# Kernel optimization log

Measured on AMD Instinct MI355X. Metric: run time of the kernel, lower is better.

The kernel has to match this reference:

```python
import jax, jax.numpy as jnp
import numpy as np

N_HEAD = 8
NEG = -1e9


def setup_inputs() -> dict:
    key = jax.random.key(0)
    ks = jax.random.split(key, 12)
    B, S, D = 16, 512, 512
    query = jax.random.normal(ks[0], (B, S, D), dtype=jnp.float32)
    inputs = jax.random.normal(ks[1], (B, S, D), dtype=jnp.float32)
    # repetition-count matrix (nonnegative ints, used via log10(x+1))
    ren_mat = jax.random.randint(ks[2], (B, S, S), 0, 10).astype(jnp.float32)
    # signed time-gap matrix (used via exp(-|t|))
    timestamp = jax.random.normal(ks[3], (B, S, S), dtype=jnp.float32) * 3.0
    # causal future mask: True above the diagonal (k=1)
    mask = jnp.triu(jnp.ones((1, S, S), dtype=bool), k=1)
    scale = 0.02
    Wq = jax.random.normal(ks[4], (D, D), dtype=jnp.float32) * scale
    Wk = jax.random.normal(ks[5], (D, D), dtype=jnp.float32) * scale
    Wv = jax.random.normal(ks[6], (D, D), dtype=jnp.float32) * scale
    Wo = jax.random.normal(ks[7], (D, D), dtype=jnp.float32) * scale
    W1 = jax.random.normal(ks[8], (D, D), dtype=jnp.float32) * scale
    bq = jnp.zeros((D,), jnp.float32); bk = jnp.zeros((D,), jnp.float32)
    bv = jnp.zeros((D,), jnp.float32); bo = jnp.zeros((D,), jnp.float32)
    b1 = jnp.zeros((D,), jnp.float32)
    ln_g = jnp.ones((D,), jnp.float32); ln_b = jnp.zeros((D,), jnp.float32)
    l1 = jax.random.uniform(ks[9], (1,), dtype=jnp.float32)  # nn.Parameter(torch.rand(1))
    gammas = jax.random.normal(ks[10], (N_HEAD, 1, 1), dtype=jnp.float32) * 0.1
    return {"query": query, "inputs": inputs, "ren_mat": ren_mat,
            "timestamp": timestamp, "mask": mask,
            "Wq": Wq, "bq": bq, "Wk": Wk, "bk": bk, "Wv": Wv, "bv": bv,
            "Wo": Wo, "bo": bo, "W1": W1, "b1": b1,
            "ln_g": ln_g, "ln_b": ln_b, "l1": l1, "gammas": gammas}


def reference(query, inputs, ren_mat, timestamp, mask,
              Wq, bq, Wk, bk, Wv, bv, Wo, bo, W1, b1, ln_g, ln_b, l1, gammas):
    B, S, D = inputs.shape
    H = N_HEAD
    hd = D // H

    def proj(x, W, b):
        # nn.Linear: x @ W.T + b, then split heads -> (B, H, S, hd)
        return (x @ W.T + b).reshape(B, S, H, hd).transpose(0, 2, 1, 3)

    q = proj(inputs, Wq, bq)
    k = proj(inputs, Wk, bk)
    v = proj(inputs, Wv, bv)

    m = mask[:, None]  # (1,1,S,S)
    # softplus(gammas) is computed in the original but unused by the math
    _ = jax.nn.softplus(gammas)

    scores = jnp.einsum('bhqd,bhkd->bhqk', q, k) / np.float32(np.sqrt(hd))
    prob_attn = jax.nn.softmax(jnp.where(m, NEG, scores), axis=-1)

    # memory-decay branch: log10 recency + exp time-decay, softmax-fused
    ren_feat = jnp.where(m, NEG, jnp.log10(ren_mat[:, None] + 1.0))   # (B,1,S,S)
    time_feat = jnp.where(m, NEG, jnp.exp(-jnp.abs(timestamp[:, None])))
    mem_attn = jax.nn.softmax(ren_feat + time_feat, axis=-1)          # (B,1,S,S)

    l = l1[0]
    p = (1.0 - l) * prob_attn + l * mem_attn  # broadcast over heads (== repeat)

    out = jnp.einsum('bhqk,bhkd->bhqd', p, v)
    out = out.transpose(0, 2, 1, 3).reshape(B, S, D)
    out = out @ Wo.T + bo            # MHA lin_out
    out = out + (out @ W1.T + b1)    # SMFE residual (dropout off in eval)
    # LayerNorm (biased variance, eps=1e-5)
    mu = out.mean(-1, keepdims=True)
    var = jnp.mean((out - mu) ** 2, axis=-1, keepdims=True)
    out = (out - mu) / jnp.sqrt(var + 1e-5) * ln_g + ln_b
    return out
```

## Files before the change

kernel.cpp:

```cpp
#include <hip/hip_runtime.h>
#include <hip/hip_bf16.h>

constexpr int B = 16, S = 512, D = 512, H = 8, HD = 64;
constexpr int BS = B * S;

typedef __attribute__((ext_vector_type(8))) short bf16x8;
typedef __attribute__((ext_vector_type(4))) float f32x4;

#define DEVI __device__ __forceinline__

DEVI bf16x8 ldbf8(const __hip_bfloat16* p) {
    return *reinterpret_cast<const bf16x8*>(p);
}

DEVI unsigned short bfbits(float f) {
    __hip_bfloat16 h = __float2bfloat16(f);
    return __builtin_bit_cast(unsigned short, h);
}

DEVI void gload_lds16(const void* g, void* l) {
    __builtin_amdgcn_global_load_lds((const __attribute__((address_space(1))) void*)g,
                                     (__attribute__((address_space(3))) void*)l, 16, 0, 0);
}

__global__ __launch_bounds__(256) void cvt_kernel(const float* __restrict__ src,
                                                  __hip_bfloat16* __restrict__ dst,
                                                  int n4) {
    int i = blockIdx.x * 256 + threadIdx.x;
    if (i >= n4) return;
    float4 v = reinterpret_cast<const float4*>(src)[i];
    unsigned int lo = (unsigned int)bfbits(v.x) | ((unsigned int)bfbits(v.y) << 16);
    unsigned int hi = (unsigned int)bfbits(v.z) | ((unsigned int)bfbits(v.w) << 16);
    uint2 o; o.x = lo; o.y = hi;
    reinterpret_cast<uint2*>(dst)[i] = o;
}

__global__ __launch_bounds__(256) void wcvt_kernel(const float* __restrict__ s0,
                                                   const float* __restrict__ s1,
                                                   const float* __restrict__ s2,
                                                   const float* __restrict__ s3,
                                                   const float* __restrict__ s4,
                                                   __hip_bfloat16* __restrict__ dst) {
    int idx = blockIdx.x * 256 + threadIdx.x;
    int wsel = idx >> 16;
    int off = idx & 65535;
    const float* s;
    switch (wsel) {
        case 0: s = s0; break;
        case 1: s = s1; break;
        case 2: s = s2; break;
        case 3: s = s3; break;
        default: s = s4; break;
    }
    float4 v = reinterpret_cast<const float4*>(s)[off];
    unsigned int lo = (unsigned int)bfbits(v.x) | ((unsigned int)bfbits(v.y) << 16);
    unsigned int hi = (unsigned int)bfbits(v.z) | ((unsigned int)bfbits(v.w) << 16);
    uint2 o; o.x = lo; o.y = hi;
    reinterpret_cast<uint2*>(dst)[idx] = o;
}

__global__ __launch_bounds__(256) void mem_attn_kernel(const float* __restrict__ ren,
                                                       const float* __restrict__ ts,
                                                       __hip_bfloat16* __restrict__ mem) {
    int tid = threadIdx.x;
    int w = tid >> 6, l = tid & 63;
    int row = blockIdx.x * 4 + w;
    int qr = row & (S - 1);
    size_t base = (size_t)row * S + l * 8;
    float f[8];
    bool active = (l * 8 <= qr);
    if (active) {
        float4 r0 = *reinterpret_cast<const float4*>(ren + base);
        float4 r1 = *reinterpret_cast<const float4*>(ren + base + 4);
        float4 t0 = *reinterpret_cast<const float4*>(ts + base);
        float4 t1 = *reinterpret_cast<const float4*>(ts + base + 4);
        float rv[8] = {r0.x, r0.y, r0.z, r0.w, r1.x, r1.y, r1.z, r1.w};
        float tv[8] = {t0.x, t0.y, t0.z, t0.w, t1.x, t1.y, t1.z, t1.w};
#pragma unroll
        for (int j = 0; j < 8; ++j) {
            int c = l * 8 + j;
            f[j] = (c <= qr) ? (__log2f(rv[j] + 1.0f) * 0.3010299957f + __expf(-fabsf(tv[j])))
                             : -3.0e38f;
        }
    } else {
#pragma unroll
        for (int j = 0; j < 8; ++j) f[j] = -3.0e38f;
    }
    float m = -3.0e38f;
#pragma unroll
    for (int j = 0; j < 8; ++j) m = fmaxf(m, f[j]);
#pragma unroll
    for (int off = 32; off >= 1; off >>= 1) m = fmaxf(m, __shfl_xor(m, off));
    float s = 0.f;
#pragma unroll
    for (int j = 0; j < 8; ++j) { float e = __expf(f[j] - m); f[j] = e; s += e; }
#pragma unroll
    for (int off = 32; off >= 1; off >>= 1) s += __shfl_xor(s, off);
    float inv = 1.0f / s;
    bf16x8 o;
#pragma unroll
    for (int j = 0; j < 8; ++j) o[j] = (short)bfbits(f[j] * inv);
    *reinterpret_cast<bf16x8*>(mem + base) = o;
}

__global__ __launch_bounds__(256) void gemm_qkv(const __hip_bfloat16* __restrict__ A,
                                                const __hip_bfloat16* __restrict__ Wqkv,
                                                const float* __restrict__ bq,
                                                const float* __restrict__ bk,
                                                const float* __restrict__ bv,
                                                __hip_bfloat16* __restrict__ q_out,
                                                __hip_bfloat16* __restrict__ k_out,
                                                __hip_bfloat16* __restrict__ vT_out) {
    constexpr int K = 512;
    int tid = threadIdx.x;
    int wv = tid >> 6, l = tid & 63;
    int wR = wv >> 1, wC = wv & 1;
    int lr = l & 15, lg = l >> 4;
    int mat = blockIdx.y >> 2;
    int rowBase = blockIdx.x * 128 + wR * 64;
    int colBase = (blockIdx.y & 3) * 128 + wC * 64;
    const float* bias = (mat == 0) ? bq : (mat == 1) ? bk : bv;
    const __hip_bfloat16* W = Wqkv + (size_t)mat * D * D;
    const __hip_bfloat16* Ab = A + (size_t)(rowBase + lr) * K + lg * 8;
    const __hip_bfloat16* Wb = W + (size_t)(colBase + lr) * K + lg * 8;

    f32x4 acc[4][4];
#pragma unroll
    for (int m = 0; m < 4; ++m)
#pragma unroll
        for (int n = 0; n < 4; ++n) acc[m][n] = (f32x4){0.f, 0.f, 0.f, 0.f};

    for (int kk = 0; kk < K; kk += 32) {
        bf16x8 a[4], b[4];
#pragma unroll
        for (int m = 0; m < 4; ++m) a[m] = ldbf8(Ab + (size_t)m * 16 * K + kk);
#pragma unroll
        for (int n = 0; n < 4; ++n) b[n] = ldbf8(Wb + (size_t)n * 16 * K + kk);
#pragma unroll
        for (int m = 0; m < 4; ++m)
#pragma unroll
            for (int n = 0; n < 4; ++n)
                acc[m][n] = __builtin_amdgcn_mfma_f32_16x16x32_bf16(a[m], b[n], acc[m][n], 0, 0, 0);
    }

#pragma unroll
    for (int n = 0; n < 4; ++n) {
        int col = colBase + n * 16 + lr;
        float bs = bias[col];
#pragma unroll
        for (int m = 0; m < 4; ++m) {
#pragma unroll
            for (int i = 0; i < 4; ++i) {
                int row = rowBase + m * 16 + lg * 4 + i;
                float val = acc[m][n][i] + bs;
                int b_ = row >> 9, s_ = row & 511, h_ = col >> 6, d_ = col & 63;
                if (mat == 2) {
                    vT_out[(((size_t)(b_ * 8 + h_) * 64 + d_) << 9) + s_] = __float2bfloat16(val);
                } else {
                    __hip_bfloat16* o = (mat == 0) ? q_out : k_out;
                    o[(((size_t)(b_ * 8 + h_) * 512 + s_) << 6) + d_] = __float2bfloat16(val);
                }
            }
        }
    }
}

template <int MODE>
__global__ __launch_bounds__(256) void gemm_bt(const __hip_bfloat16* __restrict__ A,
                                               const __hip_bfloat16* __restrict__ W,
                                               const float* __restrict__ bias,
                                               float* __restrict__ outf,
                                               __hip_bfloat16* __restrict__ outb,
                                               const float* __restrict__ resid) {
    constexpr int K = 512;
    int tid = threadIdx.x;
    int wv = tid >> 6, l = tid & 63;
    int wR = wv >> 1, wC = wv & 1;
    int lr = l & 15, lg = l >> 4;
    int rowBase = blockIdx.x * 128 + wR * 64;
    int colBase = blockIdx.y * 128 + wC * 64;
    const __hip_bfloat16* Ab = A + (size_t)(rowBase + lr) * K + lg * 8;
    const __hip_bfloat16* Wb = W + (size_t)(colBase + lr) * K + lg * 8;

    f32x4 acc[4][4];
#pragma unroll
    for (int m = 0; m < 4; ++m)
#pragma unroll
        for (int n = 0; n < 4; ++n) acc[m][n] = (f32x4){0.f, 0.f, 0.f, 0.f};

    for (int kk = 0; kk < K; kk += 32) {
        bf16x8 a[4], b[4];
#pragma unroll
        for (int m = 0; m < 4; ++m) a[m] = ldbf8(Ab + (size_t)m * 16 * K + kk);
#pragma unroll
        for (int n = 0; n < 4; ++n) b[n] = ldbf8(Wb + (size_t)n * 16 * K + kk);
#pragma unroll
        for (int m = 0; m < 4; ++m)
#pragma unroll
            for (int n = 0; n < 4; ++n)
                acc[m][n] = __builtin_amdgcn_mfma_f32_16x16x32_bf16(a[m], b[n], acc[m][n], 0, 0, 0);
    }

#pragma unroll
    for (int n = 0; n < 4; ++n) {
        int col = colBase + n * 16 + lr;
        float bs = bias[col];
#pragma unroll
        for (int m = 0; m < 4; ++m) {
#pragma unroll
            for (int i = 0; i < 4; ++i) {
                int row = rowBase + m * 16 + lg * 4 + i;
                float val = acc[m][n][i] + bs;
                size_t idx = (size_t)row * 512 + col;
                if constexpr (MODE == 2) {
                    outf[idx] = val;
                    outb[idx] = __float2bfloat16(val);
                } else {
                    outf[idx] = val + resid[idx];
                }
            }
        }
    }
}

__global__ __launch_bounds__(256) void gemm_memv(const __hip_bfloat16* __restrict__ A,
                                                 const __hip_bfloat16* __restrict__ VT,
                                                 __hip_bfloat16* __restrict__ outb) {
    int tid = threadIdx.x;
    int wv = tid >> 6, l = tid & 63;
    int wR = wv >> 1, wC = wv & 1;
    int lr = l & 15, lg = l >> 4;
    int rowBase = blockIdx.x * 128 + wR * 64;
    int colBase = blockIdx.y * 128 + wC * 64;
    int b = rowBase >> 9;
    int h = colBase >> 6;
    int klim = ((blockIdx.x & 3) + 1) * 128;

    const __hip_bfloat16* Ab = A + (size_t)(rowBase + lr) * 512 + lg * 8;
    const __hip_bfloat16* Wb = VT + ((size_t)(b * 8 + h) * 64 + lr) * 512 + lg * 8;

    f32x4 acc[4][4];
#pragma unroll
    for (int m = 0; m < 4; ++m)
#pragma unroll
        for (int n = 0; n < 4; ++n) acc[m][n] = (f32x4){0.f, 0.f, 0.f, 0.f};

    for (int kk = 0; kk < klim; kk += 32) {
        bf16x8 a[4], bb[4];
#pragma unroll
        for (int m = 0; m < 4; ++m) a[m] = ldbf8(Ab + (size_t)m * 16 * 512 + kk);
#pragma unroll
        for (int n = 0; n < 4; ++n) bb[n] = ldbf8(Wb + (size_t)n * 16 * 512 + kk);
#pragma unroll
        for (int m = 0; m < 4; ++m)
#pragma unroll
            for (int n = 0; n < 4; ++n)
                acc[m][n] = __builtin_amdgcn_mfma_f32_16x16x32_bf16(a[m], bb[n], acc[m][n], 0, 0, 0);
    }

#pragma unroll
    for (int n = 0; n < 4; ++n) {
        int col = colBase + n * 16 + lr;
#pragma unroll
        for (int m = 0; m < 4; ++m)
#pragma unroll
            for (int i = 0; i < 4; ++i) {
                int row = rowBase + m * 16 + lg * 4 + i;
                outb[(size_t)row * 512 + col] = __float2bfloat16(acc[m][n][i]);
            }
    }
}

__global__ __launch_bounds__(256, 3) void attn2_kernel(const __hip_bfloat16* __restrict__ Q,
                                                       const __hip_bfloat16* __restrict__ Km,
                                                       const __hip_bfloat16* __restrict__ VT,
                                                       const __hip_bfloat16* __restrict__ memv,
                                                       const float* __restrict__ l1,
                                                       __hip_bfloat16* __restrict__ outb) {
    __shared__ short lds[20480];
    short* Kb = lds;
    short* Vb = lds + 8192;
    int tid = threadIdx.x;
    int w = tid >> 6, l = tid & 63;
    int lr = l & 15, lg = l >> 4;
    int blk = blockIdx.x;
    int bh = blk & 127, qt = blk >> 7;
    int b = bh >> 3, h = bh & 7;
    int q0 = qt * 64;
    int nt = qt + 1;
    short* Pw = lds + 16384 + w * 1024;

    const char* Kg = (const char*)Km + (size_t)bh * 65536;
    const char* Vg = (const char*)VT + (size_t)bh * 65536;

    int o0 = w * 64 + l;
    const __hip_bfloat16* qp = Q + ((size_t)bh * 512 + q0 + w * 16 + lr) * 64 + lg * 8;
    bf16x8 qa0 = ldbf8(qp), qa1 = ldbf8(qp + 32);
    float lam = l1[0];

#pragma unroll
    for (int c = 0; c < 2; ++c) {
        int o = c * 256 + o0;
        int r = o >> 3, c16 = o & 7;
        int sw = ((c16 ^ (r & 7)) << 4);
        gload_lds16(Kg + r * 128 + sw, (char*)Kb + o * 16);
        gload_lds16(Vg + r * 1024 + sw, (char*)Vb + o * 16);
    }
    __syncthreads();

    f32x4 acc2[4];
#pragma unroll
    for (int n = 0; n < 4; ++n) acc2[n] = (f32x4){0.f, 0.f, 0.f, 0.f};
    float mrun[4] = {-3e38f, -3e38f, -3e38f, -3e38f};
    float psum[4] = {0.f, 0.f, 0.f, 0.f};

    for (int t = 0; t < nt; ++t) {
        if (t + 1 < nt) {
#pragma unroll
            for (int c = 0; c < 2; ++c) {
                int o = c * 256 + o0;
                int r = o >> 3, c16 = o & 7;
                int sw = ((c16 ^ (r & 7)) << 4);
                gload_lds16(Kg + (t + 1) * 8192 + r * 128 + sw,
                            (char*)Kb + ((t + 1) & 1) * 8192 + o * 16);
                gload_lds16(Vg + r * 1024 + (t + 1) * 128 + sw,
                            (char*)Vb + ((t + 1) & 1) * 8192 + o * 16);
            }
        }
        const short* kb = Kb + (t & 1) * 4096;
        const short* vb = Vb + (t & 1) * 4096;

        f32x4 s4[4];
#pragma unroll
        for (int j = 0; j < 4; ++j) {
            int row = j * 16 + lr;
            int sw = row & 7;
            bf16x8 k0 = *reinterpret_cast<const bf16x8*>(kb + row * 64 + ((lg ^ sw) << 3));
            bf16x8 k1 = *reinterpret_cast<const bf16x8*>(kb + row * 64 + (((4 + lg) ^ sw) << 3));
            f32x4 cc = {0.f, 0.f, 0.f, 0.f};
            cc = __builtin_amdgcn_mfma_f32_16x16x32_bf16(qa0, k0, cc, 0, 0, 0);
            cc = __builtin_amdgcn_mfma_f32_16x16x32_bf16(qa1, k1, cc, 0, 0, 0);
            s4[j] = cc;
        }

        if (t == nt - 1) {
#pragma unroll
            for (int j = 0; j < 4; ++j) {
                int col = t * 64 + j * 16 + lr;
#pragma unroll
                for (int i = 0; i < 4; ++i) {
                    int rowg = q0 + w * 16 + lg * 4 + i;
                    s4[j][i] = (col <= rowg) ? s4[j][i] * 0.125f : -3e38f;
                }
            }
        } else {
#pragma unroll
            for (int j = 0; j < 4; ++j)
#pragma unroll
                for (int i = 0; i < 4; ++i) s4[j][i] *= 0.125f;
        }

        float tmax[4];
#pragma unroll
        for (int i = 0; i < 4; ++i)
            tmax[i] = fmaxf(fmaxf(s4[0][i], s4[1][i]), fmaxf(s4[2][i], s4[3][i]));
#pragma unroll
        for (int off = 1; off < 16; off <<= 1)
#pragma unroll
            for (int i = 0; i < 4; ++i) tmax[i] = fmaxf(tmax[i], __shfl_xor(tmax[i], off));

        float e[4][4];
#pragma unroll
        for (int i = 0; i < 4; ++i) {
            float mnew = fmaxf(mrun[i], tmax[i]);
            float sc = __expf(mrun[i] - mnew);
            mrun[i] = mnew;
            float ps = 0.f;
#pragma unroll
            for (int j = 0; j < 4; ++j) {
                float ee = __expf(s4[j][i] - mnew);
                e[j][i] = ee;
                ps += ee;
            }
            psum[i] = psum[i] * sc + ps;
#pragma unroll
            for (int n = 0; n < 4; ++n) acc2[n][i] *= sc;
        }

#pragma unroll
        for (int j = 0; j < 4; ++j)
#pragma unroll
            for (int i = 0; i < 4; ++i) {
                int rr = lg * 4 + i;
                int cc = j * 16 + lr;
                Pw[rr * 64 + (cc ^ ((rr & 7) << 3))] = (short)bfbits(e[j][i]);
            }

#pragma unroll
        for (int ksub = 0; ksub < 2; ++ksub) {
            bf16x8 pa = *reinterpret_cast<const bf16x8*>(
                Pw + lr * 64 + (((ksub * 4 + lg) ^ (lr & 7)) << 3));
#pragma unroll
            for (int n = 0; n < 4; ++n) {
                int d = n * 16 + lr;
                bf16x8 vf = *reinterpret_cast<const bf16x8*>(
                    vb + d * 64 + (((ksub * 4 + lg) ^ (d & 7)) << 3));
                acc2[n] = __builtin_amdgcn_mfma_f32_16x16x32_bf16(pa, vf, acc2[n], 0, 0, 0);
            }
        }
        __syncthreads();
    }

#pragma unroll
    for (int off = 1; off < 16; off <<= 1)
#pragma unroll
        for (int i = 0; i < 4; ++i) psum[i] += __shfl_xor(psum[i], off);
    float rinv[4];
#pragma unroll
    for (int i = 0; i < 4; ++i) rinv[i] = (1.0f - lam) / psum[i];

    const __hip_bfloat16* mvp = memv + ((size_t)b * 512 + q0 + w * 16 + lg * 4) * 512 + h * 64;
    __hip_bfloat16* op = outb + ((size_t)b * 512 + q0 + w * 16 + lg * 4) * 512 + h * 64;
#pragma unroll
    for (int n = 0; n < 4; ++n)
#pragma unroll
        for (int i = 0; i < 4; ++i) {
            float mv = __bfloat162float(mvp[(size_t)i * 512 + n * 16 + lr]);
            op[(size_t)i * 512 + n * 16 + lr] =
                __float2bfloat16(acc2[n][i] * rinv[i] + lam * mv);
        }
}

__global__ __launch_bounds__(256) void ln_kernel(float* __restrict__ io,
                                                 const float* __restrict__ g,
                                                 const float* __restrict__ bb) {
    int tid = threadIdx.x;
    int w = tid >> 6, l = tid & 63;
    size_t row = (size_t)blockIdx.x * 4 + w;
    float* p = io + row * 512 + l * 8;
    float4 x0 = *reinterpret_cast<float4*>(p);
    float4 x1 = *reinterpret_cast<float4*>(p + 4);
    float xs[8] = {x0.x, x0.y, x0.z, x0.w, x1.x, x1.y, x1.z, x1.w};
    float s = 0.f;
#pragma unroll
    for (int j = 0; j < 8; ++j) s += xs[j];
#pragma unroll
    for (int off = 32; off >= 1; off >>= 1) s += __shfl_xor(s, off);
    float mu = s * (1.0f / 512.0f);
    float vs = 0.f;
#pragma unroll
    for (int j = 0; j < 8; ++j) { float d = xs[j] - mu; vs += d * d; }
#pragma unroll
    for (int off = 32; off >= 1; off >>= 1) vs += __shfl_xor(vs, off);
    float rstd = rsqrtf(vs * (1.0f / 512.0f) + 1e-5f);
    const float4 g0 = *reinterpret_cast<const float4*>(g + l * 8);
    const float4 g1 = *reinterpret_cast<const float4*>(g + l * 8 + 4);
    const float4 b0 = *reinterpret_cast<const float4*>(bb + l * 8);
    const float4 b1 = *reinterpret_cast<const float4*>(bb + l * 8 + 4);
    float gs[8] = {g0.x, g0.y, g0.z, g0.w, g1.x, g1.y, g1.z, g1.w};
    float bs[8] = {b0.x, b0.y, b0.z, b0.w, b1.x, b1.y, b1.z, b1.w};
    float ys[8];
#pragma unroll
    for (int j = 0; j < 8; ++j) ys[j] = (xs[j] - mu) * rstd * gs[j] + bs[j];
    float4 y0 = make_float4(ys[0], ys[1], ys[2], ys[3]);
    float4 y1 = make_float4(ys[4], ys[5], ys[6], ys[7]);
    *reinterpret_cast<float4*>(p) = y0;
    *reinterpret_cast<float4*>(p + 4) = y1;
}

extern "C" void kernel_launch(void* const* d_in, const int* in_sizes, int n_in,
                              void* d_out, int out_size, void* d_ws, size_t ws_size,
                              hipStream_t stream) {
    const float* inputs = (const float*)d_in[1];
    const float* ren    = (const float*)d_in[2];
    const float* ts     = (const float*)d_in[3];
    const float* Wq = (const float*)d_in[5];
    const float* bq = (const float*)d_in[6];
    const float* Wk = (const float*)d_in[7];
    const float* bk = (const float*)d_in[8];
    const float* Wv = (const float*)d_in[9];
    const float* bv = (const float*)d_in[10];
    const float* Wo = (const float*)d_in[11];
    const float* bo = (const float*)d_in[12];
    const float* W1 = (const float*)d_in[13];
    const float* b1 = (const float*)d_in[14];
    const float* ln_g = (const float*)d_in[15];
    const float* ln_b = (const float*)d_in[16];
    const float* l1   = (const float*)d_in[17];
    float* out = (float*)d_out;

    char* ws = (char*)d_ws;
    __hip_bfloat16* in_bf = (__hip_bfloat16*)(ws + 0);
    __hip_bfloat16* ao_bf = (__hip_bfloat16*)(ws + 0);
    __hip_bfloat16* wq_bf = (__hip_bfloat16*)(ws + 8388608);
    __hip_bfloat16* wo_bf = (__hip_bfloat16*)(ws + 9961472);
    __hip_bfloat16* w1_bf = (__hip_bfloat16*)(ws + 10485760);
    __hip_bfloat16* q_bf  = (__hip_bfloat16*)(ws + 11010048);
    __hip_bfloat16* o1_bf = (__hip_bfloat16*)(ws + 11010048);
    __hip_bfloat16* k_bf  = (__hip_bfloat16*)(ws + 19398656);
    __hip_bfloat16* vT_bf = (__hip_bfloat16*)(ws + 27787264);
    __hip_bfloat16* mem_bf = (__hip_bfloat16*)(ws + 36175872);
    float*          out1_f = (float*)(ws + 36175872);
    __hip_bfloat16* memv_bf = (__hip_bfloat16*)(ws + 69730304);

    cvt_kernel<<<4096, 256, 0, stream>>>(inputs, in_bf, BS * D / 4);
    wcvt_kernel<<<1280, 256, 0, stream>>>(Wq, Wk, Wv, Wo, W1, wq_bf);

    gemm_qkv<<<dim3(64, 12), 256, 0, stream>>>(in_bf, wq_bf, bq, bk, bv, q_bf, k_bf, vT_bf);

    mem_attn_kernel<<<BS / 4, 256, 0, stream>>>(ren, ts, mem_bf);

    gemm_memv<<<dim3(64, 4), 256, 0, stream>>>(mem_bf, vT_bf, memv_bf);

    attn2_kernel<<<1024, 256, 0, stream>>>(q_bf, k_bf, vT_bf, memv_bf, l1, ao_bf);

    gemm_bt<2><<<dim3(64, 4), 256, 0, stream>>>(ao_bf, wo_bf, bo, out1_f, o1_bf, nullptr);

    gemm_bt<3><<<dim3(64, 4), 256, 0, stream>>>(o1_bf, w1_bf, b1, out, nullptr, out1_f);

    ln_kernel<<<BS / 4, 256, 0, stream>>>(out, ln_g, ln_b);
}
```

Baseline: 287.9 us.

## Stage GEMM tiles through double-buffered LDS and vectorize epilogue stores via swizzled LDS

Replaces the direct-from-global MFMA operand loads in the QKV, memv, out-projection and FFN GEMMs with a shared mainloop. It stages 128x32 A and W tiles into double-buffered LDS using global_load_lds, so all four waves share the data instead of each fetching its own. The QKV and memv epilogues now write results through an XOR-swizzled LDS scratch and emit 16-byte vector stores, including the transposed V layout, instead of scattered 2-byte stores. This adds LDS usage and a barrier per k-step, which may reduce occupancy.

Result: faster. 257.3 us (-10.6%).

```diff
diff --git a/kernel.cpp b/kernel.cpp
--- a/kernel.cpp
+++ b/kernel.cpp
@@ -103,26 +103,68 @@
     *reinterpret_cast<bf16x8*>(mem + base) = o;
 }
 
-__global__ __launch_bounds__(256) void gemm_qkv(const __hip_bfloat16* __restrict__ A,
-                                                const __hip_bfloat16* __restrict__ Wqkv,
-                                                const float* __restrict__ bq,
-                                                const float* __restrict__ bk,
-                                                const float* __restrict__ bv,
-                                                __hip_bfloat16* __restrict__ q_out,
-                                                __hip_bfloat16* __restrict__ k_out,
-                                                __hip_bfloat16* __restrict__ vT_out) {
-    constexpr int K = 512;
-    int tid = threadIdx.x;
-    int wv = tid >> 6, l = tid & 63;
-    int wR = wv >> 1, wC = wv & 1;
-    int lr = l & 15, lg = l >> 4;
+
+DEVI void stage_tiles(const __hip_bfloat16* __restrict__ A,
+                      const __hip_bfloat16* __restrict__ W,
+                      int rowBase, int colBase, int kt, short* ldsbuf, int tid) {
+#pragma unroll
+    for (int c = 0; c < 2; ++c) {
+        int o = c * 256 + tid;
+        int row = o & 127, ch = o >> 7;
+        gload_lds16(A + (size_t)(rowBase + row) * 512 + kt * 32 + ch * 8,
+                    (char*)ldsbuf + o * 16);
+        gload_lds16(W + (size_t)(colBase + row) * 512 + kt * 32 + ch * 8,
+                    (char*)ldsbuf + 8192 + o * 16);
+    }
+}
+
+DEVI void gemm_mainloop(const __hip_bfloat16* __restrict__ A,
+                        const __hip_bfloat16* __restrict__ W,
+                        int rowBase, int colBase, int ktiles,
+                        short* lds, f32x4 (&acc)[4][4]) {
+    int tid = threadIdx.x;
+    int w = tid >> 6, l = tid & 63, lr = l & 15, lg = l >> 4;
+    int wR = w >> 1, wC = w & 1;
+    stage_tiles(A, W, rowBase, colBase, 0, lds, tid);
+    __syncthreads();
+    for (int t = 0; t < ktiles; ++t) {
+        if (t + 1 < ktiles)
+            stage_tiles(A, W, rowBase, colBase, t + 1, lds + ((t + 1) & 1) * 8192, tid);
+        const short* ab = lds + (t & 1) * 8192;
+        const short* bb = ab + 4096;
+        bf16x8 af[4], bfr[4];
+#pragma unroll
+        for (int m = 0; m < 4; ++m)
+            af[m] = *reinterpret_cast<const bf16x8*>(ab + (lg * 128 + wR * 64 + m * 16 + lr) * 8);
+#pragma unroll
+        for (int n = 0; n < 4; ++n)
+            bfr[n] = *reinterpret_cast<const bf16x8*>(bb + (lg * 128 + wC * 64 + n * 16 + lr) * 8);
+#pragma unroll
+        for (int m = 0; m < 4; ++m)
+#pragma unroll
+            for (int n = 0; n < 4; ++n)
+                acc[m][n] = __builtin_amdgcn_mfma_f32_16x16x32_bf16(af[m], bfr[n], acc[m][n], 0, 0, 0);
+        __syncthreads();
+    }
+}
+
+__global__ __launch_bounds__(256) void gemm_qkv_s(const __hip_bfloat16* __restrict__ A,
+                                                  const __hip_bfloat16* __restrict__ Wqkv,
+                                                  const float* __restrict__ bq,
+                                                  const float* __restrict__ bk,
+                                                  const float* __restrict__ bv,
+                                                  __hip_bfloat16* __restrict__ q_out,
+                                                  __hip_bfloat16* __restrict__ k_out,
+                                                  __hip_bfloat16* __restrict__ vT_out) {
+    __shared__ short lds[16384];
+    int tid = threadIdx.x;
+    int w = tid >> 6, l = tid & 63, lr = l & 15, lg = l >> 4;
+    int wR = w >> 1, wC = w & 1;
     int mat = blockIdx.y >> 2;
-    int rowBase = blockIdx.x * 128 + wR * 64;
-    int colBase = (blockIdx.y & 3) * 128 + wC * 64;
+    int rowBase = blockIdx.x * 128;
+    int colBase = (blockIdx.y & 3) * 128;
     const float* bias = (mat == 0) ? bq : (mat == 1) ? bk : bv;
-    const __hip_bfloat16* W = Wqkv + (size_t)mat * D * D;
-    const __hip_bfloat16* Ab = A + (size_t)(rowBase + lr) * K + lg * 8;
-    const __hip_bfloat16* Wb = W + (size_t)(colBase + lr) * K + lg * 8;
+    const __hip_bfloat16* W = Wqkv + (size_t)mat * 262144;
 
     f32x4 acc[4][4];
 #pragma unroll
@@ -130,86 +172,85 @@
 #pragma unroll
         for (int n = 0; n < 4; ++n) acc[m][n] = (f32x4){0.f, 0.f, 0.f, 0.f};
 
-    for (int kk = 0; kk < K; kk += 32) {
-        bf16x8 a[4], b[4];
-#pragma unroll
-        for (int m = 0; m < 4; ++m) a[m] = ldbf8(Ab + (size_t)m * 16 * K + kk);
-#pragma unroll
-        for (int n = 0; n < 4; ++n) b[n] = ldbf8(Wb + (size_t)n * 16 * K + kk);
+    gemm_mainloop(A, W, rowBase, colBase, 16, lds, acc);
+    short* ep = lds + w * 4096;
+    float bsv[4];
+#pragma unroll
+    for (int n = 0; n < 4; ++n) bsv[n] = bias[colBase + wC * 64 + n * 16 + lr];
+
+    if (mat < 2) {
+        __hip_bfloat16* o = (mat == 0) ? q_out : k_out;
 #pragma unroll
         for (int m = 0; m < 4; ++m)
 #pragma unroll
             for (int n = 0; n < 4; ++n)
-                acc[m][n] = __builtin_amdgcn_mfma_f32_16x16x32_bf16(a[m], b[n], acc[m][n], 0, 0, 0);
-    }
+#pragma unroll
+                for (int i = 0; i < 4; ++i) {
+                    int rr = m * 16 + lg * 4 + i, cl = n * 16 + lr;
+                    ep[rr * 64 + (cl ^ ((rr & 7) << 3))] = (short)bfbits(acc[m][n][i] + bsv[n]);
+                }
+        int h_ = (colBase + wC * 64) >> 6;
+#pragma unroll
+        for (int p = 0; p < 8; ++p) {
+            int rr = p * 8 + (l >> 3), ch = l & 7;
+            bf16x8 v = *reinterpret_cast<const bf16x8*>(ep + rr * 64 + ((ch ^ (rr & 7)) << 3));
+            int grow = rowBase + wR * 64 + rr;
+            int b_ = grow >> 9, s_ = grow & 511;
+            *reinterpret_cast<bf16x8*>(o + (((size_t)(b_ * 8 + h_) * 512 + s_) << 6) + ch * 8) = v;
+        }
+    } else {
+#pragma unroll
+        for (int m = 0; m < 4; ++m)
+#pragma unroll
+            for (int n = 0; n < 4; ++n)
+#pragma unroll
+                for (int i = 0; i < 4; ++i) {
+                    int ss = m * 16 + lg * 4 + i, dd = n * 16 + lr;
+                    ep[dd * 64 + (ss ^ ((dd & 7) << 3))] = (short)bfbits(acc[m][n][i] + bsv[n]);
+                }
+        int h_ = (colBase + wC * 64) >> 6;
+        int s0g = rowBase + wR * 64;
+        int b_ = s0g >> 9, sb = s0g & 511;
+#pragma unroll
+        for (int p = 0; p < 8; ++p) {
+            int dd = p * 8 + (l >> 3), ch = l & 7;
+            bf16x8 v = *reinterpret_cast<const bf16x8*>(ep + dd * 64 + ((ch ^ (dd & 7)) << 3));
+            *reinterpret_cast<bf16x8*>(vT_out + (((size_t)(b_ * 8 + h_) * 64 + dd) << 9) + sb + ch * 8) = v;
+        }
+    }
+}
+
+template <int MODE>
+__global__ __launch_bounds__(256) void gemm_bt_s(const __hip_bfloat16* __restrict__ A,
+                                                 const __hip_bfloat16* __restrict__ W,
+                                                 const float* __restrict__ bias,
+                                                 float* __restrict__ outf,
+                                                 __hip_bfloat16* __restrict__ outb,
+                                                 const float* __restrict__ resid) {
+    __shared__ short lds[16384];
+    int tid = threadIdx.x;
+    int w = tid >> 6, l = tid & 63, lr = l & 15, lg = l >> 4;
+    int wR = w >> 1, wC = w & 1;
+    int rowBase = blockIdx.x * 128;
+    int colBase = blockIdx.y * 128;
+
+    f32x4 acc[4][4];
+#pragma unroll
+    for (int m = 0; m < 4; ++m)
+#pragma unroll
+        for (int n = 0; n < 4; ++n) acc[m][n] = (f32x4){0.f, 0.f, 0.f, 0.f};
+
+    gemm_mainloop(A, W, rowBase, colBase, 16, lds, acc);
 
 #pragma unroll
     for (int n = 0; n < 4; ++n) {
-        int col = colBase + n * 16 + lr;
+        int col = colBase + wC * 64 + n * 16 + lr;
         float bs = bias[col];
 #pragma unroll
         for (int m = 0; m < 4; ++m) {
 #pragma unroll
             for (int i = 0; i < 4; ++i) {
-                int row = rowBase + m * 16 + lg * 4 + i;
-                float val = acc[m][n][i] + bs;
-                int b_ = row >> 9, s_ = row & 511, h_ = col >> 6, d_ = col & 63;
-                if (mat == 2) {
-                    vT_out[(((size_t)(b_ * 8 + h_) * 64 + d_) << 9) + s_] = __float2bfloat16(val);
-                } else {
-                    __hip_bfloat16* o = (mat == 0) ? q_out : k_out;
-                    o[(((size_t)(b_ * 8 + h_) * 512 + s_) << 6) + d_] = __float2bfloat16(val);
-                }
-            }
-        }
-    }
-}
-
-template <int MODE>
-__global__ __launch_bounds__(256) void gemm_bt(const __hip_bfloat16* __restrict__ A,
-                                               const __hip_bfloat16* __restrict__ W,
-                                               const float* __restrict__ bias,
-                                               float* __restrict__ outf,
-                                               __hip_bfloat16* __restrict__ outb,
-                                               const float* __restrict__ resid) {
-    constexpr int K = 512;
-    int tid = threadIdx.x;
-    int wv = tid >> 6, l = tid & 63;
-    int wR = wv >> 1, wC = wv & 1;
-    int lr = l & 15, lg = l >> 4;
-    int rowBase = blockIdx.x * 128 + wR * 64;
-    int colBase = blockIdx.y * 128 + wC * 64;
-    const __hip_bfloat16* Ab = A + (size_t)(rowBase + lr) * K + lg * 8;
-    const __hip_bfloat16* Wb = W + (size_t)(colBase + lr) * K + lg * 8;
-
-    f32x4 acc[4][4];
-#pragma unroll
-    for (int m = 0; m < 4; ++m)
-#pragma unroll
-        for (int n = 0; n < 4; ++n) acc[m][n] = (f32x4){0.f, 0.f, 0.f, 0.f};
-
-    for (int kk = 0; kk < K; kk += 32) {
-        bf16x8 a[4], b[4];
-#pragma unroll
-        for (int m = 0; m < 4; ++m) a[m] = ldbf8(Ab + (size_t)m * 16 * K + kk);
-#pragma unroll
-        for (int n = 0; n < 4; ++n) b[n] = ldbf8(Wb + (size_t)n * 16 * K + kk);
-#pragma unroll
-        for (int m = 0; m < 4; ++m)
-#pragma unroll
-            for (int n = 0; n < 4; ++n)
-                acc[m][n] = __builtin_amdgcn_mfma_f32_16x16x32_bf16(a[m], b[n], acc[m][n], 0, 0, 0);
-    }
-
-#pragma unroll
-    for (int n = 0; n < 4; ++n) {
-        int col = colBase + n * 16 + lr;
-        float bs = bias[col];
-#pragma unroll
-        for (int m = 0; m < 4; ++m) {
-#pragma unroll
-            for (int i = 0; i < 4; ++i) {
-                int row = rowBase + m * 16 + lg * 4 + i;
+                int row = rowBase + wR * 64 + m * 16 + lg * 4 + i;
                 float val = acc[m][n][i] + bs;
                 size_t idx = (size_t)row * 512 + col;
                 if constexpr (MODE == 2) {
@@ -223,21 +264,18 @@
     }
 }
 
-__global__ __launch_bounds__(256) void gemm_memv(const __hip_bfloat16* __restrict__ A,
-                                                 const __hip_bfloat16* __restrict__ VT,
-                                                 __hip_bfloat16* __restrict__ outb) {
-    int tid = threadIdx.x;
-    int wv = tid >> 6, l = tid & 63;
-    int wR = wv >> 1, wC = wv & 1;
-    int lr = l & 15, lg = l >> 4;
-    int rowBase = blockIdx.x * 128 + wR * 64;
-    int colBase = blockIdx.y * 128 + wC * 64;
-    int b = rowBase >> 9;
-    int h = colBase >> 6;
-    int klim = ((blockIdx.x & 3) + 1) * 128;
-
-    const __hip_bfloat16* Ab = A + (size_t)(rowBase + lr) * 512 + lg * 8;
-    const __hip_bfloat16* Wb = VT + ((size_t)(b * 8 + h) * 64 + lr) * 512 + lg * 8;
+__global__ __launch_bounds__(256) void gemm_memv_s(const __hip_bfloat16* __restrict__ A,
+                                                   const __hip_bfloat16* __restrict__ VT,
+                                                   __hip_bfloat16* __restrict__ outb) {
+    __shared__ short lds[16384];
+    int tid = threadIdx.x;
+    int w = tid >> 6, l = tid & 63, lr = l & 15, lg = l >> 4;
+    int wR = w >> 1, wC = w & 1;
+    int rowBase = blockIdx.x * 128;
+    int colBase = blockIdx.y * 128;
+    int b_ = rowBase >> 9;
+    const __hip_bfloat16* W = VT + (size_t)b_ * 262144;
+    int ktiles = ((blockIdx.x & 3) + 1) * 4;
 
     f32x4 acc[4][4];
 #pragma unroll
@@ -245,29 +283,24 @@
 #pragma unroll
         for (int n = 0; n < 4; ++n) acc[m][n] = (f32x4){0.f, 0.f, 0.f, 0.f};
 
-    for (int kk = 0; kk < klim; kk += 32) {
-        bf16x8 a[4], bb[4];
-#pragma unroll
-        for (int m = 0; m < 4; ++m) a[m] = ldbf8(Ab + (size_t)m * 16 * 512 + kk);
-#pragma unroll
-        for (int n = 0; n < 4; ++n) bb[n] = ldbf8(Wb + (size_t)n * 16 * 512 + kk);
-#pragma unroll
-        for (int m = 0; m < 4; ++m)
-#pragma unroll
-            for (int n = 0; n < 4; ++n)
-                acc[m][n] = __builtin_amdgcn_mfma_f32_16x16x32_bf16(a[m], bb[n], acc[m][n], 0, 0, 0);
-    }
-
-#pragma unroll
-    for (int n = 0; n < 4; ++n) {
-        int col = colBase + n * 16 + lr;
-#pragma unroll
-        for (int m = 0; m < 4; ++m)
+    gemm_mainloop(A, W, rowBase, colBase, ktiles, lds, acc);
+
+    short* ep = lds + w * 4096;
+#pragma unroll
+    for (int m = 0; m < 4; ++m)
+#pragma unroll
+        for (int n = 0; n < 4; ++n)
 #pragma unroll
             for (int i = 0; i < 4; ++i) {
-                int row = rowBase + m * 16 + lg * 4 + i;
-                outb[(size_t)row * 512 + col] = __float2bfloat16(acc[m][n][i]);
-            }
+                int rr = m * 16 + lg * 4 + i, cl = n * 16 + lr;
+                ep[rr * 64 + (cl ^ ((rr & 7) << 3))] = (short)bfbits(acc[m][n][i]);
+            }
+#pragma unroll
+    for (int p = 0; p < 8; ++p) {
+        int rr = p * 8 + (l >> 3), ch = l & 7;
+        bf16x8 v = *reinterpret_cast<const bf16x8*>(ep + rr * 64 + ((ch ^ (rr & 7)) << 3));
+        int grow = rowBase + wR * 64 + rr;
+        *reinterpret_cast<bf16x8*>(outb + (size_t)grow * 512 + colBase + wC * 64 + ch * 8) = v;
     }
 }
 
@@ -506,17 +539,17 @@
     cvt_kernel<<<4096, 256, 0, stream>>>(inputs, in_bf, BS * D / 4);
     wcvt_kernel<<<1280, 256, 0, stream>>>(Wq, Wk, Wv, Wo, W1, wq_bf);
 
-    gemm_qkv<<<dim3(64, 12), 256, 0, stream>>>(in_bf, wq_bf, bq, bk, bv, q_bf, k_bf, vT_bf);
+    gemm_qkv_s<<<dim3(64, 12), 256, 0, stream>>>(in_bf, wq_bf, bq, bk, bv, q_bf, k_bf, vT_bf);
 
     mem_attn_kernel<<<BS / 4, 256, 0, stream>>>(ren, ts, mem_bf);
 
-    gemm_memv<<<dim3(64, 4), 256, 0, stream>>>(mem_bf, vT_bf, memv_bf);
+    gemm_memv_s<<<dim3(64, 4), 256, 0, stream>>>(mem_bf, vT_bf, memv_bf);
 
     attn2_kernel<<<1024, 256, 0, stream>>>(q_bf, k_bf, vT_bf, memv_bf, l1, ao_bf);
 
-    gemm_bt<2><<<dim3(64, 4), 256, 0, stream>>>(ao_bf, wo_bf, bo, out1_f, o1_bf, nullptr);
-
-    gemm_bt<3><<<dim3(64, 4), 256, 0, stream>>>(o1_bf, w1_bf, b1, out, nullptr, out1_f);
+    gemm_bt_s<2><<<dim3(64, 4), 256, 0, stream>>>(ao_bf, wo_bf, bo, out1_f, o1_bf, nullptr);
+
+    gemm_bt_s<3><<<dim3(64, 4), 256, 0, stream>>>(o1_bf, w1_bf, b1, out, nullptr, out1_f);
 
     ln_kernel<<<BS / 4, 256, 0, stream>>>(out, ln_g, ln_b);
 }
```
